# Kernel optimization log

Measured on AMD Instinct MI355X. Metric: run time of the kernel, lower is better.

The kernel has to match this reference:

```python
import jax, jax.numpy as jnp
import numpy as np
import math

SR = 96000.0
FRAME = 2048
NB = 16
GAIN_RANGE = (-24.0, 24.0)
Q_RANGE = (0.5, 16.0)
BROADBAND = (-60.0, 0.0)
HPF_R = (20.0, 500.0)
LPF_R = (5000.0, 20000.0)
SHELF_R = (50.0, 16000.0)
PEAK_R = (100.0, 15000.0)


def _dfreq(n, rng):
    lo, hi = math.log(rng[0]), math.log(rng[1])
    return jnp.exp(lo + n * (hi - lo))


def _dgain(n, rng=GAIN_RANGE):
    return rng[0] + n * (rng[1] - rng[0])


def _dq(n):
    lo, hi = math.log(Q_RANGE[0]), math.log(Q_RANGE[1])
    return jnp.exp(lo + n * (hi - lo))


def _coeffs(ftype, fc, gain_db, Q):
    # returns stacked [g, k, a1, a2, a3, m0, m1, m2], each same shape as fc
    g = jnp.clip(jnp.tan(math.pi * fc / SR), 1e-6, 100.0)
    Q = jnp.clip(Q, 0.1, 100.0)
    one = jnp.ones_like(g)
    zero = jnp.zeros_like(g)
    if ftype in ('highpass', 'lowpass'):
        k = 1.0 / Q
        a1 = 1.0 / (1.0 + g * (g + k)); a2 = g * a1; a3 = g * a2
        if ftype == 'highpass':
            m0, m1, m2 = one, -k, -one
        else:
            m0, m1, m2 = zero, zero, one
    elif ftype == 'peak':
        A = jnp.power(10.0, gain_db / 40.0)
        k = jnp.where(gain_db >= 0, 1.0 / (Q * A), A / Q)
        a1 = 1.0 / (1.0 + g * (g + k)); a2 = g * a1; a3 = g * a2
        m0, m1, m2 = one, k * (A * A - 1.0), zero
    elif ftype == 'lowshelf':
        A = jnp.power(10.0, gain_db / 40.0); sA = jnp.sqrt(A); k = 1.0 / Q
        gs = jnp.where(gain_db >= 0, g / sA, g * sA)
        a1 = 1.0 / (1.0 + gs * (gs + k)); a2 = gs * a1; a3 = gs * a2
        m0, m1, m2 = one, k * (A - 1.0), A * A - 1.0
    else:  # highshelf
        A = jnp.power(10.0, gain_db / 40.0); sA = jnp.sqrt(A); k = 1.0 / Q
        gs = jnp.where(gain_db >= 0, g * sA, g / sA)
        a1 = 1.0 / (1.0 + gs * (gs + k)); a2 = gs * a1; a3 = gs * a2
        m0, m1, m2 = A * A, k * (1.0 - A) * A, 1.0 - A * A
    return jnp.stack([g, k, a1, a2, a3, m0, m1, m2], 0)


def _all_coeffs(params, n_frames_audio):
    # params: (B, 50, n_frames_params) -> coeffs (nF, NB, 8, B), in/out gains (nF, B)
    B = params.shape[0]
    nFp = params.shape[2]
    pidx = jnp.minimum(jnp.arange(n_frames_audio), nFp - 1)
    fp = jnp.take(params, pidx, axis=2)                 # (B, 50, nF)
    bq = fp[:, :NB * 3, :].reshape(B, NB, 3, n_frames_audio)
    in_g = jnp.power(10.0, _dgain(fp[:, -2, :], BROADBAND) / 20.0)   # (B, nF)
    out_g = jnp.power(10.0, _dgain(fp[:, -1, :], BROADBAND) / 20.0)  # (B, nF)
    cs = []
    for i in range(NB):
        fn, gn, qn = bq[:, i, 0], bq[:, i, 1], bq[:, i, 2]  # (B, nF)
        Q = _dq(qn)
        if i == 0:
            c = _coeffs('highpass', _dfreq(fn, HPF_R), None, Q)
        elif i == 15:
            c = _coeffs('lowpass', _dfreq(fn, LPF_R), None, Q)
        elif i == 1:
            c = _coeffs('lowshelf', _dfreq(fn, SHELF_R), _dgain(gn), Q)
        elif i == 14:
            c = _coeffs('highshelf', _dfreq(fn, SHELF_R), _dgain(gn), Q)
        else:
            c = _coeffs('peak', _dfreq(fn, PEAK_R), _dgain(gn), Q)
        cs.append(c)  # (8, B, nF)
    coeffs = jnp.transpose(jnp.stack(cs, 0), (3, 0, 1, 2))  # (nF, NB, 8, B)
    return coeffs, in_g.T, out_g.T


def _forward(audio, params):
    B, S = audio.shape
    nF = S // FRAME  # S chosen as exact multiple of FRAME
    coeffs, in_g, out_g = _all_coeffs(params, nF)
    frames = jnp.transpose(audio.reshape(B, nF, FRAME), (1, 2, 0))  # (nF, FRAME, B)

    def frame_step(states, xs):
        fr, c, ig, og = xs  # fr (FRAME,B), c (NB,8,B), ig (B,), og (B,)
        x = fr * ig[None, :]
        new_states = []
        for i in range(NB):
            a1, a2, a3 = c[i, 2], c[i, 3], c[i, 4]
            m0, m1, m2 = c[i, 5], c[i, 6], c[i, 7]

            def samp(st, xn, a1=a1, a2=a2, a3=a3, m0=m0, m1=m1, m2=m2):
                ic1, ic2 = st
                v3 = xn - ic2
                v1 = a1 * ic1 + a2 * v3
                v2 = ic2 + a2 * v1 + a3 * v3
                out = m0 * xn + m1 * v1 + m2 * v2
                return (2.0 * v1 - ic1, 2.0 * v2 - ic2), out

            (ic1, ic2), x = jax.lax.scan(samp, (states[i, 0], states[i, 1]), x)
            new_states.append(jnp.stack([ic1, ic2], 0))
        return jnp.stack(new_states, 0), x * og[None, :]

    init = jnp.zeros((NB, 2, B), audio.dtype)
    _, out = jax.lax.scan(frame_step, init, (frames, coeffs, in_g, out_g))
    return jnp.transpose(out, (2, 0, 1)).reshape(B, S)  # (B, S)


_forward_jit = jax.jit(_forward)


def setup_inputs() -> dict:
    key = jax.random.key(0)
    k1, k2 = jax.random.split(key)
    B, S, nFp = 32, 49152, 24  # 24 frames of 2048 samples
    audio = jax.random.normal(k1, (B, S), dtype=jnp.float32) * 0.1
    params = jax.random.uniform(k2, (B, 50, nFp), dtype=jnp.float32)
    return {'audio': audio, 'params': params}


def reference(audio, params):
    return _forward_jit(audio, params)
```

## Files before the change

### kernel.cpp

```cpp
#include <hip/hip_runtime.h>
#include <math.h>

#define NBATCH 32
#define S      49152
#define NF     24
#define NB     16
#define NBLK   4
#define CHUNK  16
#define NCH    768
#define NWAVE  12

__device__ __forceinline__ float clampf(float x, float lo, float hi) {
    return fminf(fmaxf(x, lo), hi);
}

#define FOREACH_S(OP) \
    OP(s00) OP(s01) OP(s02) OP(s03) OP(s04) OP(s05) OP(s06) OP(s07) \
    OP(s08) OP(s09) OP(s10) OP(s11) OP(s12) OP(s13) OP(s14) OP(s15)

#define DECL_S(x) float x;

#define STEPA(x) { \
    const float n1_ = fmaf(t00, ic1, fmaf(t01, ic2, b0 * (x))); \
    const float n2_ = fmaf(t10, ic1, fmaf(t11, ic2, b1 * (x))); \
    ic1 = n1_; ic2 = n2_; }

#define STEPC(x) { \
    const float y_  = fmaf(c0, ic1, fmaf(c1, ic2, c2 * (x))); \
    const float n1_ = fmaf(t00, ic1, fmaf(t01, ic2, b0 * (x))); \
    const float n2_ = fmaf(t10, ic1, fmaf(t11, ic2, b1 * (x))); \
    (x) = y_; ic1 = n1_; ic2 = n2_; }

__global__ __launch_bounds__(NCH, 3)
void biquad_chain_kernel(const float* __restrict__ audio,
                         const float* __restrict__ params,
                         float* __restrict__ out,
                         unsigned int* __restrict__ ws)
{
    __shared__ float sc[NB][NF][16];
    __shared__ float sgain[2][NF];
    __shared__ float4 sincl[NB][NWAVE][2];
    __shared__ unsigned int stag[NB][NWAVE];

    const int t       = threadIdx.x;
    const int xcd     = blockIdx.x & 7;
    const int slot_   = blockIdx.x >> 3;
    const int bt      = xcd * 4 + (slot_ & 3);
    const int quarter = slot_ >> 2;
    const int lane    = t & 63;
    const int wave    = t >> 6;
    const int frame   = quarter * 6 + (wave >> 1);

    if (t < NB * NF) {
        const int f  = t / NF;
        const int fr = t % NF;
        const float* P = params + (size_t)bt * 50 * NF;
        const float fn = P[(3 * f + 0) * NF + fr];
        const float gn = P[(3 * f + 1) * NF + fr];
        const float qn = P[(3 * f + 2) * NF + fr];

        float Q = __expf(-0.69314718f + qn * 3.4657359f);
        Q = clampf(Q, 0.1f, 100.0f);

        float lo, hi;
        int type;
        if      (f == 0)  { lo = 20.0f;   hi = 500.0f;   type = 0; }
        else if (f == 15) { lo = 5000.0f; hi = 20000.0f; type = 1; }
        else if (f == 1)  { lo = 50.0f;   hi = 16000.0f; type = 3; }
        else if (f == 14) { lo = 50.0f;   hi = 16000.0f; type = 4; }
        else              { lo = 100.0f;  hi = 15000.0f; type = 2; }

        const float fc = __expf(__logf(lo) + fn * (__logf(hi) - __logf(lo)));
        float g_ = __tanf((float)M_PI * fc / 96000.0f);
        g_ = clampf(g_, 1e-6f, 100.0f);
        const float gdb = -24.0f + 48.0f * gn;

        float a1, a2, a3, m0, m1, m2;
        if (type == 0 || type == 1) {
            const float k = 1.0f / Q;
            a1 = 1.0f / (1.0f + g_ * (g_ + k)); a2 = g_ * a1; a3 = g_ * a2;
            if (type == 0) { m0 = 1.0f; m1 = -k;   m2 = -1.0f; }
            else           { m0 = 0.0f; m1 = 0.0f; m2 = 1.0f;  }
        } else if (type == 2) {
            const float A = __expf(gdb * (2.30258509f / 40.0f));
            const float k = (gdb >= 0.0f) ? 1.0f / (Q * A) : A / Q;
            a1 = 1.0f / (1.0f + g_ * (g_ + k)); a2 = g_ * a1; a3 = g_ * a2;
            m0 = 1.0f; m1 = k * (A * A - 1.0f); m2 = 0.0f;
        } else {
            const float A  = __expf(gdb * (2.30258509f / 40.0f));
            const float sA = sqrtf(A);
            const float k  = 1.0f / Q;
            float gs;
            if (type == 3) gs = (gdb >= 0.0f) ? g_ / sA : g_ * sA;
            else           gs = (gdb >= 0.0f) ? g_ * sA : g_ / sA;
            a1 = 1.0f / (1.0f + gs * (gs + k)); a2 = gs * a1; a3 = gs * a2;
            if (type == 3) { m0 = 1.0f;  m1 = k * (A - 1.0f);      m2 = A * A - 1.0f; }
            else           { m0 = A * A; m1 = k * (1.0f - A) * A;  m2 = 1.0f - A * A; }
        }

        const float q2  = a2 * a2 + a3;
        const float t00 = 2.0f * a1 - 1.0f;
        const float t01 = -2.0f * a2;
        const float t10 = 2.0f * a1 * a2;
        const float t11 = 1.0f - 2.0f * q2;
        const float b0  = 2.0f * a2;
        const float b1  = 2.0f * q2;
        const float c0  = a1 * (m1 + m2 * a2);
        const float c1  = m2 * (1.0f - q2) - m1 * a2;
        const float c2  = m0 + m1 * a2 + m2 * q2;

        float u00 = t00, u01 = t01, u10 = t10, u11 = t11;
        #pragma unroll
        for (int i = 0; i < 4; i++) {
            const float n00 = u00 * u00 + u01 * u10;
            const float n01 = u00 * u01 + u01 * u11;
            const float n10 = u10 * u00 + u11 * u10;
            const float n11 = u10 * u01 + u11 * u11;
            u00 = n00; u01 = n01; u10 = n10; u11 = n11;
        }

        sc[f][fr][0] = t00; sc[f][fr][1] = t01; sc[f][fr][2] = t10; sc[f][fr][3] = t11;
        sc[f][fr][4] = b0;  sc[f][fr][5] = b1;  sc[f][fr][6] = c0;  sc[f][fr][7] = c1;
        sc[f][fr][8] = c2;  sc[f][fr][9] = u00; sc[f][fr][10] = u01; sc[f][fr][11] = u10;
        sc[f][fr][12] = u11;
    }
    if (t >= 384 && t < 384 + 2 * NF) {
        const int idx = t - 384;
        const int which = idx / NF;
        const int fr    = idx % NF;
        const float* P = params + (size_t)bt * 50 * NF;
        const float p  = P[(48 + which) * NF + fr];
        const float db = -60.0f + 60.0f * p;
        sgain[which][fr] = __expf(db * (2.30258509f / 20.0f));
    }
    if (t < NB * NWAVE) stag[t / NWAVE][t % NWAVE] = 0u;
    __syncthreads();

    FOREACH_S(DECL_S)
    {
        const float ing = sgain[0][frame];
        const float* base = audio + (size_t)bt * S
                          + (size_t)(quarter * NCH + t) * CHUNK;
        float4 q;
        q = *(const float4*)(base +  0); s00 = q.x*ing; s01 = q.y*ing; s02 = q.z*ing; s03 = q.w*ing;
        q = *(const float4*)(base +  4); s04 = q.x*ing; s05 = q.y*ing; s06 = q.z*ing; s07 = q.w*ing;
        q = *(const float4*)(base +  8); s08 = q.x*ing; s09 = q.y*ing; s10 = q.z*ing; s11 = q.w*ing;
        q = *(const float4*)(base + 12); s12 = q.x*ing; s13 = q.y*ing; s14 = q.z*ing; s15 = q.w*ing;
    }

    #pragma unroll 1
    for (int f = 0; f < NB; f++) {
        const float4 q0 = *(const float4*)&sc[f][frame][0];
        const float4 q1 = *(const float4*)&sc[f][frame][4];
        const float4 q2 = *(const float4*)&sc[f][frame][8];
        const float  M11v = sc[f][frame][12];
        const float t00 = q0.x, t01 = q0.y, t10 = q0.z, t11 = q0.w;
        const float b0  = q1.x, b1  = q1.y, c0  = q1.z, c1  = q1.w;
        const float c2  = q2.x;

        float ic1 = 0.0f, ic2 = 0.0f;
        FOREACH_S(STEPA)

        float Md00 = q2.y, Md01 = q2.z, Md10 = q2.w, Md11 = M11v;
        float Ac0 = ic1, Ac1 = ic2;
        #pragma unroll
        for (int d = 1; d < 64; d <<= 1) {
            const float lc0 = __shfl_up(Ac0, d);
            const float lc1 = __shfl_up(Ac1, d);
            if (lane >= d) {
                Ac0 = fmaf(Md00, lc0, fmaf(Md01, lc1, Ac0));
                Ac1 = fmaf(Md10, lc0, fmaf(Md11, lc1, Ac1));
            }
            const float n00 = Md00 * Md00 + Md01 * Md10;
            const float n01 = Md00 * Md01 + Md01 * Md11;
            const float n10 = Md10 * Md00 + Md11 * Md10;
            const float n11 = Md10 * Md01 + Md11 * Md11;
            Md00 = n00; Md01 = n01; Md10 = n10; Md11 = n11;
        }

        float ce0 = __shfl_up(Ac0, 1);
        float ce1 = __shfl_up(Ac1, 1);
        if (lane == 0) { ce0 = 0.0f; ce1 = 0.0f; }

        const unsigned int tag = (unsigned int)(f + 1);
        float Mp00 = 1.0f, Mp01 = 0.0f, Mp10 = 0.0f, Mp11 = 1.0f;
        float cp0 = 0.0f, cp1 = 0.0f;
        if (wave > 0) {
            while (__hip_atomic_load(&stag[f][wave - 1], __ATOMIC_ACQUIRE,
                                     __HIP_MEMORY_SCOPE_WORKGROUP) != tag)
                __builtin_amdgcn_s_sleep(1);
            const float4 d0 = sincl[f][wave - 1][0];
            const float4 d1 = sincl[f][wave - 1][1];
            Mp00 = d0.x; Mp01 = d0.y; Mp10 = d0.z; Mp11 = d0.w;
            cp0 = d1.x; cp1 = d1.y;
        } else if (quarter > 0) {
            unsigned int* gs = ws + ((size_t)(bt * NB + f) * NBLK + (quarter - 1)) * 8;
            while (__hip_atomic_load(gs, __ATOMIC_ACQUIRE,
                                     __HIP_MEMORY_SCOPE_AGENT) != tag)
                __builtin_amdgcn_s_sleep(1);
            const float* dp = (const float*)(gs + 1);
            Mp00 = __hip_atomic_load(&dp[0], __ATOMIC_RELAXED, __HIP_MEMORY_SCOPE_AGENT);
            Mp01 = __hip_atomic_load(&dp[1], __ATOMIC_RELAXED, __HIP_MEMORY_SCOPE_AGENT);
            Mp10 = __hip_atomic_load(&dp[2], __ATOMIC_RELAXED, __HIP_MEMORY_SCOPE_AGENT);
            Mp11 = __hip_atomic_load(&dp[3], __ATOMIC_RELAXED, __HIP_MEMORY_SCOPE_AGENT);
            cp0  = __hip_atomic_load(&dp[4], __ATOMIC_RELAXED, __HIP_MEMORY_SCOPE_AGENT);
            cp1  = __hip_atomic_load(&dp[5], __ATOMIC_RELAXED, __HIP_MEMORY_SCOPE_AGENT);
        }

        if (lane == 63) {
            const float I00 = fmaf(Md00, Mp00, Md01 * Mp10);
            const float I01 = fmaf(Md00, Mp01, Md01 * Mp11);
            const float I10 = fmaf(Md10, Mp00, Md11 * Mp10);
            const float I11 = fmaf(Md10, Mp01, Md11 * Mp11);
            const float Ic0 = fmaf(Md00, cp0, fmaf(Md01, cp1, Ac0));
            const float Ic1 = fmaf(Md10, cp0, fmaf(Md11, cp1, Ac1));
            if (wave < NWAVE - 1) {
                sincl[f][wave][0] = make_float4(I00, I01, I10, I11);
                sincl[f][wave][1] = make_float4(Ic0, Ic1, 0.0f, 0.0f);
                __hip_atomic_store(&stag[f][wave], tag, __ATOMIC_RELEASE,
                                   __HIP_MEMORY_SCOPE_WORKGROUP);
            } else if (quarter < NBLK - 1) {
                unsigned int* gs = ws + ((size_t)(bt * NB + f) * NBLK + quarter) * 8;
                float* dp = (float*)(gs + 1);
                __hip_atomic_store(&dp[0], I00, __ATOMIC_RELAXED, __HIP_MEMORY_SCOPE_AGENT);
                __hip_atomic_store(&dp[1], I01, __ATOMIC_RELAXED, __HIP_MEMORY_SCOPE_AGENT);
                __hip_atomic_store(&dp[2], I10, __ATOMIC_RELAXED, __HIP_MEMORY_SCOPE_AGENT);
                __hip_atomic_store(&dp[3], I11, __ATOMIC_RELAXED, __HIP_MEMORY_SCOPE_AGENT);
                __hip_atomic_store(&dp[4], Ic0, __ATOMIC_RELAXED, __HIP_MEMORY_SCOPE_AGENT);
                __hip_atomic_store(&dp[5], Ic1, __ATOMIC_RELAXED, __HIP_MEMORY_SCOPE_AGENT);
                __hip_atomic_store(gs, tag, __ATOMIC_RELEASE, __HIP_MEMORY_SCOPE_AGENT);
            }
        }

        float w0 = cp0, w1 = cp1;
        float p00 = q2.y, p01 = q2.z, p10 = q2.w, p11 = M11v;
        #pragma unroll
        for (int b = 0; b < 6; b++) {
            if (lane & (1 << b)) {
                const float nw0 = fmaf(p00, w0, p01 * w1);
                const float nw1 = fmaf(p10, w0, p11 * w1);
                w0 = nw0; w1 = nw1;
            }
            if (b < 5) {
                const float n00 = p00 * p00 + p01 * p10;
                const float n01 = p00 * p01 + p01 * p11;
                const float n10 = p10 * p00 + p11 * p10;
                const float n11 = p10 * p01 + p11 * p11;
                p00 = n00; p01 = n01; p10 = n10; p11 = n11;
            }
        }
        ic1 = w0 + ce0;
        ic2 = w1 + ce1;

        FOREACH_S(STEPC)
    }

    {
        const float og = sgain[1][frame];
        float* base = out + (size_t)bt * S + (size_t)(quarter * NCH + t) * CHUNK;
        float4 q;
        q.x = s00*og; q.y = s01*og; q.z = s02*og; q.w = s03*og; *(float4*)(base +  0) = q;
        q.x = s04*og; q.y = s05*og; q.z = s06*og; q.w = s07*og; *(float4*)(base +  4) = q;
        q.x = s08*og; q.y = s09*og; q.z = s10*og; q.w = s11*og; *(float4*)(base +  8) = q;
        q.x = s12*og; q.y = s13*og; q.z = s14*og; q.w = s15*og; *(float4*)(base + 12) = q;
    }
}

extern "C" void kernel_launch(void* const* d_in, const int* in_sizes, int n_in,
                              void* d_out, int out_size, void* d_ws, size_t ws_size,
                              hipStream_t stream)
{
    const float* audio  = (const float*)d_in[0];
    const float* params = (const float*)d_in[1];
    float* out = (float*)d_out;
    unsigned int* ws = (unsigned int*)d_ws;
    biquad_chain_kernel<<<NBLK * NBATCH, NCH, 0, stream>>>(audio, params, out, ws);
}
```

Before: 123.1 us.

## Replace serial wave/block carry chain with decoupled aggregate lookback scan

Each wave now publishes only its local affine aggregate (matrix plus offset) to shared memory, then folds all earlier waves' aggregates itself. The previous scheme waited on the predecessor's inclusive prefix, which serialised the chain across waves. Across blocks, the last wave publishes the block aggregate and wave 0 of later blocks folds all preceding blocks' aggregates, then shares the resulting state with its other waves. This is meant to cut the serial dependency latency at the cost of redundant matrix folds, more polling, and the inter-block chain still being waited on.

```diff
diff --git a/kernel.cpp b/kernel.cpp
--- a/kernel.cpp
+++ b/kernel.cpp
@@ -39,8 +39,11 @@
 {
     __shared__ float sc[NB][NF][16];
     __shared__ float sgain[2][NF];
-    __shared__ float4 sincl[NB][NWAVE][2];
-    __shared__ unsigned int stag[NB][NWAVE];
+    __shared__ float4 swaggM[NB][NWAVE];
+    __shared__ float2 swaggC[NB][NWAVE];
+    __shared__ unsigned int swtag[NB][NWAVE];
+    __shared__ float2 sblk[NB];
+    __shared__ unsigned int sblktag[NB];
 
     const int t       = threadIdx.x;
     const int xcd     = blockIdx.x & 7;
@@ -133,7 +136,8 @@
         const float db = -60.0f + 60.0f * p;
         sgain[which][fr] = __expf(db * (2.30258509f / 20.0f));
     }
-    if (t < NB * NWAVE) stag[t / NWAVE][t % NWAVE] = 0u;
+    if (t < NB * NWAVE) swtag[t / NWAVE][t % NWAVE] = 0u;
+    if (t < NB) sblktag[t] = 0u;
     __syncthreads();
 
     FOREACH_S(DECL_S)
@@ -183,56 +187,89 @@
         if (lane == 0) { ce0 = 0.0f; ce1 = 0.0f; }
 
         const unsigned int tag = (unsigned int)(f + 1);
-        float Mp00 = 1.0f, Mp01 = 0.0f, Mp10 = 0.0f, Mp11 = 1.0f;
-        float cp0 = 0.0f, cp1 = 0.0f;
-        if (wave > 0) {
-            while (__hip_atomic_load(&stag[f][wave - 1], __ATOMIC_ACQUIRE,
+
+        if (lane == 63) {
+            swaggM[f][wave] = make_float4(Md00, Md01, Md10, Md11);
+            swaggC[f][wave] = make_float2(Ac0, Ac1);
+            __hip_atomic_store(&swtag[f][wave], tag, __ATOMIC_RELEASE,
+                               __HIP_MEMORY_SCOPE_WORKGROUP);
+        }
+
+        float F00 = 1.0f, F01 = 0.0f, F10 = 0.0f, F11 = 1.0f;
+        float Fc0 = 0.0f, Fc1 = 0.0f;
+        for (int j = 0; j < wave; j++) {
+            while (__hip_atomic_load(&swtag[f][j], __ATOMIC_ACQUIRE,
                                      __HIP_MEMORY_SCOPE_WORKGROUP) != tag)
                 __builtin_amdgcn_s_sleep(1);
-            const float4 d0 = sincl[f][wave - 1][0];
-            const float4 d1 = sincl[f][wave - 1][1];
-            Mp00 = d0.x; Mp01 = d0.y; Mp10 = d0.z; Mp11 = d0.w;
-            cp0 = d1.x; cp1 = d1.y;
-        } else if (quarter > 0) {
-            unsigned int* gs = ws + ((size_t)(bt * NB + f) * NBLK + (quarter - 1)) * 8;
-            while (__hip_atomic_load(gs, __ATOMIC_ACQUIRE,
-                                     __HIP_MEMORY_SCOPE_AGENT) != tag)
-                __builtin_amdgcn_s_sleep(1);
-            const float* dp = (const float*)(gs + 1);
-            Mp00 = __hip_atomic_load(&dp[0], __ATOMIC_RELAXED, __HIP_MEMORY_SCOPE_AGENT);
-            Mp01 = __hip_atomic_load(&dp[1], __ATOMIC_RELAXED, __HIP_MEMORY_SCOPE_AGENT);
-            Mp10 = __hip_atomic_load(&dp[2], __ATOMIC_RELAXED, __HIP_MEMORY_SCOPE_AGENT);
-            Mp11 = __hip_atomic_load(&dp[3], __ATOMIC_RELAXED, __HIP_MEMORY_SCOPE_AGENT);
-            cp0  = __hip_atomic_load(&dp[4], __ATOMIC_RELAXED, __HIP_MEMORY_SCOPE_AGENT);
-            cp1  = __hip_atomic_load(&dp[5], __ATOMIC_RELAXED, __HIP_MEMORY_SCOPE_AGENT);
-        }
-
-        if (lane == 63) {
-            const float I00 = fmaf(Md00, Mp00, Md01 * Mp10);
-            const float I01 = fmaf(Md00, Mp01, Md01 * Mp11);
-            const float I10 = fmaf(Md10, Mp00, Md11 * Mp10);
-            const float I11 = fmaf(Md10, Mp01, Md11 * Mp11);
-            const float Ic0 = fmaf(Md00, cp0, fmaf(Md01, cp1, Ac0));
-            const float Ic1 = fmaf(Md10, cp0, fmaf(Md11, cp1, Ac1));
-            if (wave < NWAVE - 1) {
-                sincl[f][wave][0] = make_float4(I00, I01, I10, I11);
-                sincl[f][wave][1] = make_float4(Ic0, Ic1, 0.0f, 0.0f);
-                __hip_atomic_store(&stag[f][wave], tag, __ATOMIC_RELEASE,
-                                   __HIP_MEMORY_SCOPE_WORKGROUP);
-            } else if (quarter < NBLK - 1) {
+            const float4 m = swaggM[f][j];
+            const float2 c = swaggC[f][j];
+            const float n00 = fmaf(m.x, F00, m.y * F10);
+            const float n01 = fmaf(m.x, F01, m.y * F11);
+            const float n10 = fmaf(m.z, F00, m.w * F10);
+            const float n11 = fmaf(m.z, F01, m.w * F11);
+            const float nc0 = fmaf(m.x, Fc0, fmaf(m.y, Fc1, c.x));
+            const float nc1 = fmaf(m.z, Fc0, fmaf(m.w, Fc1, c.y));
+            F00 = n00; F01 = n01; F10 = n10; F11 = n11;
+            Fc0 = nc0; Fc1 = nc1;
+        }
+
+        if (wave == NWAVE - 1 && quarter < NBLK - 1) {
+            const float B00 = fmaf(Md00, F00, Md01 * F10);
+            const float B01 = fmaf(Md00, F01, Md01 * F11);
+            const float B10 = fmaf(Md10, F00, Md11 * F10);
+            const float B11 = fmaf(Md10, F01, Md11 * F11);
+            const float Bc0 = fmaf(Md00, Fc0, fmaf(Md01, Fc1, Ac0));
+            const float Bc1 = fmaf(Md10, Fc0, fmaf(Md11, Fc1, Ac1));
+            if (lane == 63) {
                 unsigned int* gs = ws + ((size_t)(bt * NB + f) * NBLK + quarter) * 8;
                 float* dp = (float*)(gs + 1);
-                __hip_atomic_store(&dp[0], I00, __ATOMIC_RELAXED, __HIP_MEMORY_SCOPE_AGENT);
-                __hip_atomic_store(&dp[1], I01, __ATOMIC_RELAXED, __HIP_MEMORY_SCOPE_AGENT);
-                __hip_atomic_store(&dp[2], I10, __ATOMIC_RELAXED, __HIP_MEMORY_SCOPE_AGENT);
-                __hip_atomic_store(&dp[3], I11, __ATOMIC_RELAXED, __HIP_MEMORY_SCOPE_AGENT);
-                __hip_atomic_store(&dp[4], Ic0, __ATOMIC_RELAXED, __HIP_MEMORY_SCOPE_AGENT);
-                __hip_atomic_store(&dp[5], Ic1, __ATOMIC_RELAXED, __HIP_MEMORY_SCOPE_AGENT);
+                __hip_atomic_store(&dp[0], B00, __ATOMIC_RELAXED, __HIP_MEMORY_SCOPE_AGENT);
+                __hip_atomic_store(&dp[1], B01, __ATOMIC_RELAXED, __HIP_MEMORY_SCOPE_AGENT);
+                __hip_atomic_store(&dp[2], B10, __ATOMIC_RELAXED, __HIP_MEMORY_SCOPE_AGENT);
+                __hip_atomic_store(&dp[3], B11, __ATOMIC_RELAXED, __HIP_MEMORY_SCOPE_AGENT);
+                __hip_atomic_store(&dp[4], Bc0, __ATOMIC_RELAXED, __HIP_MEMORY_SCOPE_AGENT);
+                __hip_atomic_store(&dp[5], Bc1, __ATOMIC_RELAXED, __HIP_MEMORY_SCOPE_AGENT);
                 __hip_atomic_store(gs, tag, __ATOMIC_RELEASE, __HIP_MEMORY_SCOPE_AGENT);
             }
         }
 
-        float w0 = cp0, w1 = cp1;
+        float Sbx = 0.0f, Sby = 0.0f;
+        if (quarter > 0) {
+            if (wave == 0) {
+                for (int k = 0; k < quarter; k++) {
+                    unsigned int* gs = ws + ((size_t)(bt * NB + f) * NBLK + k) * 8;
+                    while (__hip_atomic_load(gs, __ATOMIC_ACQUIRE,
+                                             __HIP_MEMORY_SCOPE_AGENT) != tag)
+                        __builtin_amdgcn_s_sleep(1);
+                    const float* dp = (const float*)(gs + 1);
+                    const float m00 = __hip_atomic_load(&dp[0], __ATOMIC_RELAXED, __HIP_MEMORY_SCOPE_AGENT);
+                    const float m01 = __hip_atomic_load(&dp[1], __ATOMIC_RELAXED, __HIP_MEMORY_SCOPE_AGENT);
+                    const float m10 = __hip_atomic_load(&dp[2], __ATOMIC_RELAXED, __HIP_MEMORY_SCOPE_AGENT);
+                    const float m11 = __hip_atomic_load(&dp[3], __ATOMIC_RELAXED, __HIP_MEMORY_SCOPE_AGENT);
+                    const float cc0 = __hip_atomic_load(&dp[4], __ATOMIC_RELAXED, __HIP_MEMORY_SCOPE_AGENT);
+                    const float cc1 = __hip_atomic_load(&dp[5], __ATOMIC_RELAXED, __HIP_MEMORY_SCOPE_AGENT);
+                    const float nx = fmaf(m00, Sbx, fmaf(m01, Sby, cc0));
+                    const float ny = fmaf(m10, Sbx, fmaf(m11, Sby, cc1));
+                    Sbx = nx; Sby = ny;
+                }
+                if (lane == 0) {
+                    sblk[f] = make_float2(Sbx, Sby);
+                    __hip_atomic_store(&sblktag[f], tag, __ATOMIC_RELEASE,
+                                       __HIP_MEMORY_SCOPE_WORKGROUP);
+                }
+            } else {
+                while (__hip_atomic_load(&sblktag[f], __ATOMIC_ACQUIRE,
+                                         __HIP_MEMORY_SCOPE_WORKGROUP) != tag)
+                    __builtin_amdgcn_s_sleep(1);
+                const float2 sb = sblk[f];
+                Sbx = sb.x; Sby = sb.y;
+            }
+        }
+
+        const float vx = fmaf(F00, Sbx, fmaf(F01, Sby, Fc0));
+        const float vy = fmaf(F10, Sbx, fmaf(F11, Sby, Fc1));
+
+        float w0 = vx, w1 = vy;
         float p00 = q2.y, p01 = q2.z, p10 = q2.w, p11 = M11v;
         #pragma unroll
         for (int b = 0; b < 6; b++) {
```

Result: slower. 138.2 us (+12.3%).

## Map one wave per frame and pass only state vectors between frames

Applied to the files above, without the earlier changes.

Restructures the chunked-scan biquad kernel so each wave handles one whole 2048-sample frame (32 samples per lane), with 4 waves per block and 6 blocks per batch item. Each block now computes coefficients only for its own 4 frames. Because coefficients change at frame boundaries, only the 2-element state needs to pass between waves and blocks, so the 2x2 transfer-matrix composition and the larger handoff payloads go away. In exchange, each lane holds more registers for 32 samples, the serial sequential work per lane doubles, and the cross-block dependency chain gets longer (6 blocks instead of 4).

```diff
diff --git a/kernel.cpp b/kernel.cpp
--- a/kernel.cpp
+++ b/kernel.cpp
@@ -5,10 +5,10 @@
 #define S      49152
 #define NF     24
 #define NB     16
-#define NBLK   4
-#define CHUNK  16
-#define NCH    768
-#define NWAVE  12
+#define CHUNK  32
+#define NWPB   4
+#define NBLKF  6
+#define NCH    256
 
 __device__ __forceinline__ float clampf(float x, float lo, float hi) {
     return fminf(fmaxf(x, lo), hi);
@@ -16,7 +16,9 @@
 
 #define FOREACH_S(OP) \
     OP(s00) OP(s01) OP(s02) OP(s03) OP(s04) OP(s05) OP(s06) OP(s07) \
-    OP(s08) OP(s09) OP(s10) OP(s11) OP(s12) OP(s13) OP(s14) OP(s15)
+    OP(s08) OP(s09) OP(s10) OP(s11) OP(s12) OP(s13) OP(s14) OP(s15) \
+    OP(s16) OP(s17) OP(s18) OP(s19) OP(s20) OP(s21) OP(s22) OP(s23) \
+    OP(s24) OP(s25) OP(s26) OP(s27) OP(s28) OP(s29) OP(s30) OP(s31)
 
 #define DECL_S(x) float x;
 
@@ -31,87 +33,94 @@
     const float n2_ = fmaf(t10, ic1, fmaf(t11, ic2, b1 * (x))); \
     (x) = y_; ic1 = n1_; ic2 = n2_; }
 
-__global__ __launch_bounds__(NCH, 3)
+struct Aff { float t00, t01, t10, t11, b0, b1, c0, c1, c2; };
+
+__device__ __forceinline__ Aff biquad_affine(int f, const float* P, int fr) {
+    const float fn = P[(3 * f + 0) * NF + fr];
+    const float gn = P[(3 * f + 1) * NF + fr];
+    const float qn = P[(3 * f + 2) * NF + fr];
+
+    float Q = __expf(-0.69314718f + qn * 3.4657359f);
+    Q = clampf(Q, 0.1f, 100.0f);
+
+    float lo, hi;
+    int type;
+    if      (f == 0)  { lo = 20.0f;   hi = 500.0f;   type = 0; }
+    else if (f == 15) { lo = 5000.0f; hi = 20000.0f; type = 1; }
+    else if (f == 1)  { lo = 50.0f;   hi = 16000.0f; type = 3; }
+    else if (f == 14) { lo = 50.0f;   hi = 16000.0f; type = 4; }
+    else              { lo = 100.0f;  hi = 15000.0f; type = 2; }
+
+    const float fc = __expf(__logf(lo) + fn * (__logf(hi) - __logf(lo)));
+    float g_ = __tanf((float)M_PI * fc / 96000.0f);
+    g_ = clampf(g_, 1e-6f, 100.0f);
+    const float gdb = -24.0f + 48.0f * gn;
+
+    float a1, a2, a3, m0, m1, m2;
+    if (type == 0 || type == 1) {
+        const float k = 1.0f / Q;
+        a1 = 1.0f / (1.0f + g_ * (g_ + k)); a2 = g_ * a1; a3 = g_ * a2;
+        if (type == 0) { m0 = 1.0f; m1 = -k;   m2 = -1.0f; }
+        else           { m0 = 0.0f; m1 = 0.0f; m2 = 1.0f;  }
+    } else if (type == 2) {
+        const float A = __expf(gdb * (2.30258509f / 40.0f));
+        const float k = (gdb >= 0.0f) ? 1.0f / (Q * A) : A / Q;
+        a1 = 1.0f / (1.0f + g_ * (g_ + k)); a2 = g_ * a1; a3 = g_ * a2;
+        m0 = 1.0f; m1 = k * (A * A - 1.0f); m2 = 0.0f;
+    } else {
+        const float A  = __expf(gdb * (2.30258509f / 40.0f));
+        const float sA = sqrtf(A);
+        const float k  = 1.0f / Q;
+        float gs;
+        if (type == 3) gs = (gdb >= 0.0f) ? g_ / sA : g_ * sA;
+        else           gs = (gdb >= 0.0f) ? g_ * sA : g_ / sA;
+        a1 = 1.0f / (1.0f + gs * (gs + k)); a2 = gs * a1; a3 = gs * a2;
+        if (type == 3) { m0 = 1.0f;  m1 = k * (A - 1.0f);      m2 = A * A - 1.0f; }
+        else           { m0 = A * A; m1 = k * (1.0f - A) * A;  m2 = 1.0f - A * A; }
+    }
+
+    const float q2 = a2 * a2 + a3;
+    Aff r;
+    r.t00 = 2.0f * a1 - 1.0f;
+    r.t01 = -2.0f * a2;
+    r.t10 = 2.0f * a1 * a2;
+    r.t11 = 1.0f - 2.0f * q2;
+    r.b0  = 2.0f * a2;
+    r.b1  = 2.0f * q2;
+    r.c0  = a1 * (m1 + m2 * a2);
+    r.c1  = m2 * (1.0f - q2) - m1 * a2;
+    r.c2  = m0 + m1 * a2 + m2 * q2;
+    return r;
+}
+
+__global__ __launch_bounds__(NCH, 2)
 void biquad_chain_kernel(const float* __restrict__ audio,
                          const float* __restrict__ params,
                          float* __restrict__ out,
                          unsigned int* __restrict__ ws)
 {
-    __shared__ float sc[NB][NF][16];
-    __shared__ float sgain[2][NF];
-    __shared__ float4 sincl[NB][NWAVE][2];
-    __shared__ unsigned int stag[NB][NWAVE];
-
-    const int t       = threadIdx.x;
-    const int xcd     = blockIdx.x & 7;
-    const int slot_   = blockIdx.x >> 3;
-    const int bt      = xcd * 4 + (slot_ & 3);
-    const int quarter = slot_ >> 2;
-    const int lane    = t & 63;
-    const int wave    = t >> 6;
-    const int frame   = quarter * 6 + (wave >> 1);
-
-    if (t < NB * NF) {
-        const int f  = t / NF;
-        const int fr = t % NF;
+    __shared__ float scf[NWPB][NB][16];
+    __shared__ float sgain[2][NWPB];
+    __shared__ float sst[NWPB - 1][NB][2];
+    __shared__ unsigned int stag[NWPB - 1][NB];
+
+    const int t    = threadIdx.x;
+    const int bt   = blockIdx.x & 31;
+    const int blk  = blockIdx.x >> 5;
+    const int lane = t & 63;
+    const int wave = t >> 6;
+    const int frg  = blk * NWPB + wave;
+
+    if (t < NWPB * NB) {
+        const int f   = t & 15;
+        const int frl = t >> 4;
+        const int fr  = blk * NWPB + frl;
         const float* P = params + (size_t)bt * 50 * NF;
-        const float fn = P[(3 * f + 0) * NF + fr];
-        const float gn = P[(3 * f + 1) * NF + fr];
-        const float qn = P[(3 * f + 2) * NF + fr];
-
-        float Q = __expf(-0.69314718f + qn * 3.4657359f);
-        Q = clampf(Q, 0.1f, 100.0f);
-
-        float lo, hi;
-        int type;
-        if      (f == 0)  { lo = 20.0f;   hi = 500.0f;   type = 0; }
-        else if (f == 15) { lo = 5000.0f; hi = 20000.0f; type = 1; }
-        else if (f == 1)  { lo = 50.0f;   hi = 16000.0f; type = 3; }
-        else if (f == 14) { lo = 50.0f;   hi = 16000.0f; type = 4; }
-        else              { lo = 100.0f;  hi = 15000.0f; type = 2; }
-
-        const float fc = __expf(__logf(lo) + fn * (__logf(hi) - __logf(lo)));
-        float g_ = __tanf((float)M_PI * fc / 96000.0f);
-        g_ = clampf(g_, 1e-6f, 100.0f);
-        const float gdb = -24.0f + 48.0f * gn;
-
-        float a1, a2, a3, m0, m1, m2;
-        if (type == 0 || type == 1) {
-            const float k = 1.0f / Q;
-            a1 = 1.0f / (1.0f + g_ * (g_ + k)); a2 = g_ * a1; a3 = g_ * a2;
-            if (type == 0) { m0 = 1.0f; m1 = -k;   m2 = -1.0f; }
-            else           { m0 = 0.0f; m1 = 0.0f; m2 = 1.0f;  }
-        } else if (type == 2) {
-            const float A = __expf(gdb * (2.30258509f / 40.0f));
-            const float k = (gdb >= 0.0f) ? 1.0f / (Q * A) : A / Q;
-            a1 = 1.0f / (1.0f + g_ * (g_ + k)); a2 = g_ * a1; a3 = g_ * a2;
-            m0 = 1.0f; m1 = k * (A * A - 1.0f); m2 = 0.0f;
-        } else {
-            const float A  = __expf(gdb * (2.30258509f / 40.0f));
-            const float sA = sqrtf(A);
-            const float k  = 1.0f / Q;
-            float gs;
-            if (type == 3) gs = (gdb >= 0.0f) ? g_ / sA : g_ * sA;
-            else           gs = (gdb >= 0.0f) ? g_ * sA : g_ / sA;
-            a1 = 1.0f / (1.0f + gs * (gs + k)); a2 = gs * a1; a3 = gs * a2;
-            if (type == 3) { m0 = 1.0f;  m1 = k * (A - 1.0f);      m2 = A * A - 1.0f; }
-            else           { m0 = A * A; m1 = k * (1.0f - A) * A;  m2 = 1.0f - A * A; }
-        }
-
-        const float q2  = a2 * a2 + a3;
-        const float t00 = 2.0f * a1 - 1.0f;
-        const float t01 = -2.0f * a2;
-        const float t10 = 2.0f * a1 * a2;
-        const float t11 = 1.0f - 2.0f * q2;
-        const float b0  = 2.0f * a2;
-        const float b1  = 2.0f * q2;
-        const float c0  = a1 * (m1 + m2 * a2);
-        const float c1  = m2 * (1.0f - q2) - m1 * a2;
-        const float c2  = m0 + m1 * a2 + m2 * q2;
-
-        float u00 = t00, u01 = t01, u10 = t10, u11 = t11;
+        const Aff A = biquad_affine(f, P, fr);
+
+        float u00 = A.t00, u01 = A.t01, u10 = A.t10, u11 = A.t11;
         #pragma unroll
-        for (int i = 0; i < 4; i++) {
+        for (int i = 0; i < 5; i++) {
             const float n00 = u00 * u00 + u01 * u10;
             const float n01 = u00 * u01 + u01 * u11;
             const float n10 = u10 * u00 + u11 * u10;
@@ -119,41 +128,48 @@
             u00 = n00; u01 = n01; u10 = n10; u11 = n11;
         }
 
-        sc[f][fr][0] = t00; sc[f][fr][1] = t01; sc[f][fr][2] = t10; sc[f][fr][3] = t11;
-        sc[f][fr][4] = b0;  sc[f][fr][5] = b1;  sc[f][fr][6] = c0;  sc[f][fr][7] = c1;
-        sc[f][fr][8] = c2;  sc[f][fr][9] = u00; sc[f][fr][10] = u01; sc[f][fr][11] = u10;
-        sc[f][fr][12] = u11;
-    }
-    if (t >= 384 && t < 384 + 2 * NF) {
-        const int idx = t - 384;
-        const int which = idx / NF;
-        const int fr    = idx % NF;
-        const float* P = params + (size_t)bt * 50 * NF;
-        const float p  = P[(48 + which) * NF + fr];
-        const float db = -60.0f + 60.0f * p;
-        sgain[which][fr] = __expf(db * (2.30258509f / 20.0f));
-    }
-    if (t < NB * NWAVE) stag[t / NWAVE][t % NWAVE] = 0u;
+        float* d = scf[frl][f];
+        d[0] = A.t00; d[1] = A.t01; d[2]  = A.t10; d[3]  = A.t11;
+        d[4] = A.b0;  d[5] = A.b1;  d[6]  = A.c0;  d[7]  = A.c1;
+        d[8] = A.c2;  d[9] = u00;   d[10] = u01;   d[11] = u10;
+        d[12] = u11;
+    }
+    if (t >= 64 && t < 64 + 2 * NWPB) {
+        const int idx   = t - 64;
+        const int which = idx >> 2;
+        const int frl   = idx & 3;
+        const int fr    = blk * NWPB + frl;
+        const float* P  = params + (size_t)bt * 50 * NF;
+        const float p   = P[(48 + which) * NF + fr];
+        const float db  = -60.0f + 60.0f * p;
+        sgain[which][frl] = __expf(db * (2.30258509f / 20.0f));
+    }
+    if (t < (NWPB - 1) * NB) stag[t / NB][t % NB] = 0u;
     __syncthreads();
 
     FOREACH_S(DECL_S)
     {
-        const float ing = sgain[0][frame];
-        const float* base = audio + (size_t)bt * S
-                          + (size_t)(quarter * NCH + t) * CHUNK;
+        const float ing = sgain[0][wave];
+        const float* base = audio + (size_t)bt * S + (size_t)frg * 2048
+                          + (size_t)lane * CHUNK;
         float4 q;
         q = *(const float4*)(base +  0); s00 = q.x*ing; s01 = q.y*ing; s02 = q.z*ing; s03 = q.w*ing;
         q = *(const float4*)(base +  4); s04 = q.x*ing; s05 = q.y*ing; s06 = q.z*ing; s07 = q.w*ing;
         q = *(const float4*)(base +  8); s08 = q.x*ing; s09 = q.y*ing; s10 = q.z*ing; s11 = q.w*ing;
         q = *(const float4*)(base + 12); s12 = q.x*ing; s13 = q.y*ing; s14 = q.z*ing; s15 = q.w*ing;
+        q = *(const float4*)(base + 16); s16 = q.x*ing; s17 = q.y*ing; s18 = q.z*ing; s19 = q.w*ing;
+        q = *(const float4*)(base + 20); s20 = q.x*ing; s21 = q.y*ing; s22 = q.z*ing; s23 = q.w*ing;
+        q = *(const float4*)(base + 24); s24 = q.x*ing; s25 = q.y*ing; s26 = q.z*ing; s27 = q.w*ing;
+        q = *(const float4*)(base + 28); s28 = q.x*ing; s29 = q.y*ing; s30 = q.z*ing; s31 = q.w*ing;
     }
 
     #pragma unroll 1
     for (int f = 0; f < NB; f++) {
-        const float4 q0 = *(const float4*)&sc[f][frame][0];
-        const float4 q1 = *(const float4*)&sc[f][frame][4];
-        const float4 q2 = *(const float4*)&sc[f][frame][8];
-        const float  M11v = sc[f][frame][12];
+        const float* d = scf[wave][f];
+        const float4 q0 = *(const float4*)(d + 0);
+        const float4 q1 = *(const float4*)(d + 4);
+        const float4 q2 = *(const float4*)(d + 8);
+        const float  M11v = d[12];
         const float t00 = q0.x, t01 = q0.y, t10 = q0.z, t11 = q0.w;
         const float b0  = q1.x, b1  = q1.y, c0  = q1.z, c1  = q1.w;
         const float c2  = q2.x;
@@ -164,10 +180,10 @@
         float Md00 = q2.y, Md01 = q2.z, Md10 = q2.w, Md11 = M11v;
         float Ac0 = ic1, Ac1 = ic2;
         #pragma unroll
-        for (int d = 1; d < 64; d <<= 1) {
-            const float lc0 = __shfl_up(Ac0, d);
-            const float lc1 = __shfl_up(Ac1, d);
-            if (lane >= d) {
+        for (int dd = 1; dd < 64; dd <<= 1) {
+            const float lc0 = __shfl_up(Ac0, dd);
+            const float lc1 = __shfl_up(Ac1, dd);
+            if (lane >= dd) {
                 Ac0 = fmaf(Md00, lc0, fmaf(Md01, lc1, Ac0));
                 Ac1 = fmaf(Md10, lc0, fmaf(Md11, lc1, Ac1));
             }
@@ -183,56 +199,47 @@
         if (lane == 0) { ce0 = 0.0f; ce1 = 0.0f; }
 
         const unsigned int tag = (unsigned int)(f + 1);
-        float Mp00 = 1.0f, Mp01 = 0.0f, Mp10 = 0.0f, Mp11 = 1.0f;
-        float cp0 = 0.0f, cp1 = 0.0f;
-        if (wave > 0) {
-            while (__hip_atomic_load(&stag[f][wave - 1], __ATOMIC_ACQUIRE,
-                                     __HIP_MEMORY_SCOPE_WORKGROUP) != tag)
-                __builtin_amdgcn_s_sleep(1);
-            const float4 d0 = sincl[f][wave - 1][0];
-            const float4 d1 = sincl[f][wave - 1][1];
-            Mp00 = d0.x; Mp01 = d0.y; Mp10 = d0.z; Mp11 = d0.w;
-            cp0 = d1.x; cp1 = d1.y;
-        } else if (quarter > 0) {
-            unsigned int* gs = ws + ((size_t)(bt * NB + f) * NBLK + (quarter - 1)) * 8;
-            while (__hip_atomic_load(gs, __ATOMIC_ACQUIRE,
-                                     __HIP_MEMORY_SCOPE_AGENT) != tag)
-                __builtin_amdgcn_s_sleep(1);
-            const float* dp = (const float*)(gs + 1);
-            Mp00 = __hip_atomic_load(&dp[0], __ATOMIC_RELAXED, __HIP_MEMORY_SCOPE_AGENT);
-            Mp01 = __hip_atomic_load(&dp[1], __ATOMIC_RELAXED, __HIP_MEMORY_SCOPE_AGENT);
-            Mp10 = __hip_atomic_load(&dp[2], __ATOMIC_RELAXED, __HIP_MEMORY_SCOPE_AGENT);
-            Mp11 = __hip_atomic_load(&dp[3], __ATOMIC_RELAXED, __HIP_MEMORY_SCOPE_AGENT);
-            cp0  = __hip_atomic_load(&dp[4], __ATOMIC_RELAXED, __HIP_MEMORY_SCOPE_AGENT);
-            cp1  = __hip_atomic_load(&dp[5], __ATOMIC_RELAXED, __HIP_MEMORY_SCOPE_AGENT);
-        }
-
-        if (lane == 63) {
-            const float I00 = fmaf(Md00, Mp00, Md01 * Mp10);
-            const float I01 = fmaf(Md00, Mp01, Md01 * Mp11);
-            const float I10 = fmaf(Md10, Mp00, Md11 * Mp10);
-            const float I11 = fmaf(Md10, Mp01, Md11 * Mp11);
-            const float Ic0 = fmaf(Md00, cp0, fmaf(Md01, cp1, Ac0));
-            const float Ic1 = fmaf(Md10, cp0, fmaf(Md11, cp1, Ac1));
-            if (wave < NWAVE - 1) {
-                sincl[f][wave][0] = make_float4(I00, I01, I10, I11);
-                sincl[f][wave][1] = make_float4(Ic0, Ic1, 0.0f, 0.0f);
-                __hip_atomic_store(&stag[f][wave], tag, __ATOMIC_RELEASE,
+        float v0 = 0.0f, v1 = 0.0f;
+        if (frg > 0) {
+            if (wave > 0) {
+                while (__hip_atomic_load(&stag[wave - 1][f], __ATOMIC_ACQUIRE,
+                                         __HIP_MEMORY_SCOPE_WORKGROUP) != tag)
+                    __builtin_amdgcn_s_sleep(1);
+                v0 = sst[wave - 1][f][0];
+                v1 = sst[wave - 1][f][1];
+            } else {
+                unsigned int* gs = ws + ((size_t)(bt * (NBLKF - 1) + (blk - 1)) * NB + f) * 4;
+                if (lane == 0) {
+                    while (__hip_atomic_load(gs, __ATOMIC_ACQUIRE,
+                                             __HIP_MEMORY_SCOPE_AGENT) != tag)
+                        __builtin_amdgcn_s_sleep(1);
+                    const float* dp = (const float*)(gs + 1);
+                    v0 = __hip_atomic_load(&dp[0], __ATOMIC_RELAXED, __HIP_MEMORY_SCOPE_AGENT);
+                    v1 = __hip_atomic_load(&dp[1], __ATOMIC_RELAXED, __HIP_MEMORY_SCOPE_AGENT);
+                }
+                v0 = __shfl(v0, 0);
+                v1 = __shfl(v1, 0);
+            }
+        }
+
+        if (lane == 63 && frg < NF - 1) {
+            const float o0 = fmaf(Md00, v0, fmaf(Md01, v1, Ac0));
+            const float o1 = fmaf(Md10, v0, fmaf(Md11, v1, Ac1));
+            if (wave < NWPB - 1) {
+                sst[wave][f][0] = o0;
+                sst[wave][f][1] = o1;
+                __hip_atomic_store(&stag[wave][f], tag, __ATOMIC_RELEASE,
                                    __HIP_MEMORY_SCOPE_WORKGROUP);
-            } else if (quarter < NBLK - 1) {
-                unsigned int* gs = ws + ((size_t)(bt * NB + f) * NBLK + quarter) * 8;
+            } else {
+                unsigned int* gs = ws + ((size_t)(bt * (NBLKF - 1) + blk) * NB + f) * 4;
                 float* dp = (float*)(gs + 1);
-                __hip_atomic_store(&dp[0], I00, __ATOMIC_RELAXED, __HIP_MEMORY_SCOPE_AGENT);
-                __hip_atomic_store(&dp[1], I01, __ATOMIC_RELAXED, __HIP_MEMORY_SCOPE_AGENT);
-                __hip_atomic_store(&dp[2], I10, __ATOMIC_RELAXED, __HIP_MEMORY_SCOPE_AGENT);
-                __hip_atomic_store(&dp[3], I11, __ATOMIC_RELAXED, __HIP_MEMORY_SCOPE_AGENT);
-                __hip_atomic_store(&dp[4], Ic0, __ATOMIC_RELAXED, __HIP_MEMORY_SCOPE_AGENT);
-                __hip_atomic_store(&dp[5], Ic1, __ATOMIC_RELAXED, __HIP_MEMORY_SCOPE_AGENT);
+                __hip_atomic_store(&dp[0], o0, __ATOMIC_RELAXED, __HIP_MEMORY_SCOPE_AGENT);
+                __hip_atomic_store(&dp[1], o1, __ATOMIC_RELAXED, __HIP_MEMORY_SCOPE_AGENT);
                 __hip_atomic_store(gs, tag, __ATOMIC_RELEASE, __HIP_MEMORY_SCOPE_AGENT);
             }
         }
 
-        float w0 = cp0, w1 = cp1;
+        float w0 = v0, w1 = v1;
         float p00 = q2.y, p01 = q2.z, p10 = q2.w, p11 = M11v;
         #pragma unroll
         for (int b = 0; b < 6; b++) {
@@ -256,13 +263,18 @@
     }
 
     {
-        const float og = sgain[1][frame];
-        float* base = out + (size_t)bt * S + (size_t)(quarter * NCH + t) * CHUNK;
+        const float og = sgain[1][wave];
+        float* base = out + (size_t)bt * S + (size_t)frg * 2048
+                    + (size_t)lane * CHUNK;
         float4 q;
         q.x = s00*og; q.y = s01*og; q.z = s02*og; q.w = s03*og; *(float4*)(base +  0) = q;
         q.x = s04*og; q.y = s05*og; q.z = s06*og; q.w = s07*og; *(float4*)(base +  4) = q;
         q.x = s08*og; q.y = s09*og; q.z = s10*og; q.w = s11*og; *(float4*)(base +  8) = q;
         q.x = s12*og; q.y = s13*og; q.z = s14*og; q.w = s15*og; *(float4*)(base + 12) = q;
+        q.x = s16*og; q.y = s17*og; q.z = s18*og; q.w = s19*og; *(float4*)(base + 16) = q;
+        q.x = s20*og; q.y = s21*og; q.z = s22*og; q.w = s23*og; *(float4*)(base + 20) = q;
+        q.x = s24*og; q.y = s25*og; q.z = s26*og; q.w = s27*og; *(float4*)(base + 24) = q;
+        q.x = s28*og; q.y = s29*og; q.z = s30*og; q.w = s31*og; *(float4*)(base + 28) = q;
     }
 }
 
@@ -274,5 +286,5 @@
     const float* params = (const float*)d_in[1];
     float* out = (float*)d_out;
     unsigned int* ws = (unsigned int*)d_ws;
-    biquad_chain_kernel<<<NBLK * NBATCH, NCH, 0, stream>>>(audio, params, out, ws);
-}
+    biquad_chain_kernel<<<NBLKF * NBATCH, NCH, 0, stream>>>(audio, params, out, ws);
+}
```

After: 147.4 us. +19.8%, slower.

## Replace serial wave-chained state scan with precomputed transition matrices and single-wave combine

Applied to the files above, without the earlier changes.

Precomputes per-wave and per-quarter transition-matrix powers in shared memory during setup, so the per-filter cross-wave combine becomes a block barrier plus one wave doing a short serial affine scan over the wave aggregates. Blocks now publish only a 2-float carry vector instead of a full matrix plus vector, and each block reads all earlier blocks' carries in parallel instead of waiting on a chain. This removes the wave-to-wave and block-to-block serial spin-wait chain. In exchange it adds a __syncthreads per filter stage, more shared memory and setup work, and it relies on the piecewise-constant frame structure to precompute the matrices.

```diff
diff --git a/kernel.cpp b/kernel.cpp
--- a/kernel.cpp
+++ b/kernel.cpp
@@ -38,9 +38,14 @@
                          unsigned int* __restrict__ ws)
 {
     __shared__ float sc[NB][NF][16];
+    __shared__ float sT2048[NB][NF][4];
+    __shared__ float sMw[NB][NWAVE][4];
+    __shared__ float sPm[NB][NWAVE][4];
+    __shared__ float sWm[NB][3][4];
     __shared__ float sgain[2][NF];
-    __shared__ float4 sincl[NB][NWAVE][2];
-    __shared__ unsigned int stag[NB][NWAVE];
+    __shared__ float sagg[2][NWAVE][2];
+    __shared__ float sv[NWAVE][2];
+    __shared__ unsigned int sflag[NB];
 
     const int t       = threadIdx.x;
     const int xcd     = blockIdx.x & 7;
@@ -118,11 +123,34 @@
             const float n11 = u10 * u01 + u11 * u11;
             u00 = n00; u01 = n01; u10 = n10; u11 = n11;
         }
-
         sc[f][fr][0] = t00; sc[f][fr][1] = t01; sc[f][fr][2] = t10; sc[f][fr][3] = t11;
         sc[f][fr][4] = b0;  sc[f][fr][5] = b1;  sc[f][fr][6] = c0;  sc[f][fr][7] = c1;
         sc[f][fr][8] = c2;  sc[f][fr][9] = u00; sc[f][fr][10] = u01; sc[f][fr][11] = u10;
         sc[f][fr][12] = u11;
+
+        #pragma unroll
+        for (int i = 0; i < 6; i++) {
+            const float n00 = u00 * u00 + u01 * u10;
+            const float n01 = u00 * u01 + u01 * u11;
+            const float n10 = u10 * u00 + u11 * u10;
+            const float n11 = u10 * u01 + u11 * u11;
+            u00 = n00; u01 = n01; u10 = n10; u11 = n11;
+        }
+        const int lf = fr - quarter * 6;
+        if (lf >= 0 && lf < 6) {
+            sMw[f][2 * lf][0] = u00; sMw[f][2 * lf][1] = u01;
+            sMw[f][2 * lf][2] = u10; sMw[f][2 * lf][3] = u11;
+            sMw[f][2 * lf + 1][0] = u00; sMw[f][2 * lf + 1][1] = u01;
+            sMw[f][2 * lf + 1][2] = u10; sMw[f][2 * lf + 1][3] = u11;
+        }
+        {
+            const float n00 = u00 * u00 + u01 * u10;
+            const float n01 = u00 * u01 + u01 * u11;
+            const float n10 = u10 * u00 + u11 * u10;
+            const float n11 = u10 * u01 + u11 * u11;
+            sT2048[f][fr][0] = n00; sT2048[f][fr][1] = n01;
+            sT2048[f][fr][2] = n10; sT2048[f][fr][3] = n11;
+        }
     }
     if (t >= 384 && t < 384 + 2 * NF) {
         const int idx = t - 384;
@@ -133,7 +161,56 @@
         const float db = -60.0f + 60.0f * p;
         sgain[which][fr] = __expf(db * (2.30258509f / 20.0f));
     }
-    if (t < NB * NWAVE) stag[t / NWAVE][t % NWAVE] = 0u;
+    if (t < NB) sflag[t] = 0u;
+    __syncthreads();
+
+    if (t < NB) {
+        const int f = t;
+        float q00 = 1.0f, q01 = 0.0f, q10 = 0.0f, q11 = 1.0f;
+        #pragma unroll
+        for (int k = 0; k < 6; k++) {
+            sPm[f][2 * k][0] = q00; sPm[f][2 * k][1] = q01;
+            sPm[f][2 * k][2] = q10; sPm[f][2 * k][3] = q11;
+            const float m00 = sMw[f][2 * k][0], m01 = sMw[f][2 * k][1];
+            const float m10 = sMw[f][2 * k][2], m11 = sMw[f][2 * k][3];
+            sPm[f][2 * k + 1][0] = m00 * q00 + m01 * q10;
+            sPm[f][2 * k + 1][1] = m00 * q01 + m01 * q11;
+            sPm[f][2 * k + 1][2] = m10 * q00 + m11 * q10;
+            sPm[f][2 * k + 1][3] = m10 * q01 + m11 * q11;
+            const float g00 = sT2048[f][quarter * 6 + k][0], g01 = sT2048[f][quarter * 6 + k][1];
+            const float g10 = sT2048[f][quarter * 6 + k][2], g11 = sT2048[f][quarter * 6 + k][3];
+            const float n00 = g00 * q00 + g01 * q10;
+            const float n01 = g00 * q01 + g01 * q11;
+            const float n10 = g10 * q00 + g11 * q10;
+            const float n11 = g10 * q01 + g11 * q11;
+            q00 = n00; q01 = n01; q10 = n10; q11 = n11;
+        }
+        if (quarter > 0) {
+            float r00 = 1.0f, r01 = 0.0f, r10 = 0.0f, r11 = 1.0f;
+            for (int k = quarter - 1; k >= 0; k--) {
+                sWm[f][k][0] = r00; sWm[f][k][1] = r01;
+                sWm[f][k][2] = r10; sWm[f][k][3] = r11;
+                if (k > 0) {
+                    float b00 = 1.0f, b01 = 0.0f, b10 = 0.0f, b11 = 1.0f;
+                    #pragma unroll
+                    for (int m = 0; m < 6; m++) {
+                        const float g00 = sT2048[f][6 * k + m][0], g01 = sT2048[f][6 * k + m][1];
+                        const float g10 = sT2048[f][6 * k + m][2], g11 = sT2048[f][6 * k + m][3];
+                        const float n00 = g00 * b00 + g01 * b10;
+                        const float n01 = g00 * b01 + g01 * b11;
+                        const float n10 = g10 * b00 + g11 * b10;
+                        const float n11 = g10 * b01 + g11 * b11;
+                        b00 = n00; b01 = n01; b10 = n10; b11 = n11;
+                    }
+                    const float n00 = r00 * b00 + r01 * b10;
+                    const float n01 = r00 * b01 + r01 * b11;
+                    const float n10 = r10 * b00 + r11 * b10;
+                    const float n11 = r10 * b01 + r11 * b11;
+                    r00 = n00; r01 = n01; r10 = n10; r11 = n11;
+                }
+            }
+        }
+    }
     __syncthreads();
 
     FOREACH_S(DECL_S)
@@ -178,61 +255,85 @@
             Md00 = n00; Md01 = n01; Md10 = n10; Md11 = n11;
         }
 
+        const int buf = f & 1;
+        if (lane == 63) {
+            sagg[buf][wave][0] = Ac0;
+            sagg[buf][wave][1] = Ac1;
+        }
+        __syncthreads();
+
+        const unsigned int tag = (unsigned int)(f + 1);
+        unsigned int* stagebase = ws + ((size_t)(bt * NB + f) * NBLK) * 8;
+
+        if (wave == 0) {
+            float Pc0 = 0.0f, Pc1 = 0.0f;
+            #pragma unroll
+            for (int j = 0; j < NWAVE; j++) {
+                const float a0 = sagg[buf][j][0];
+                const float a1v = sagg[buf][j][1];
+                const float m00 = sMw[f][j][0], m01 = sMw[f][j][1];
+                const float m10 = sMw[f][j][2], m11 = sMw[f][j][3];
+                if (lane > j) {
+                    const float n0 = fmaf(m00, Pc0, fmaf(m01, Pc1, a0));
+                    const float n1 = fmaf(m10, Pc0, fmaf(m11, Pc1, a1v));
+                    Pc0 = n0; Pc1 = n1;
+                }
+            }
+
+            if (quarter < NBLK - 1 && lane == NWAVE) {
+                unsigned int* slot = stagebase + quarter * 8;
+                float* dp = (float*)(slot + 1);
+                __hip_atomic_store(&dp[0], Pc0, __ATOMIC_RELAXED, __HIP_MEMORY_SCOPE_AGENT);
+                __hip_atomic_store(&dp[1], Pc1, __ATOMIC_RELAXED, __HIP_MEMORY_SCOPE_AGENT);
+                __hip_atomic_store(slot, tag, __ATOMIC_RELEASE, __HIP_MEMORY_SCOPE_AGENT);
+            }
+
+            float S0x = 0.0f, S0y = 0.0f;
+            if (quarter > 0) {
+                float ux = 0.0f, uy = 0.0f;
+                if (lane < quarter) {
+                    unsigned int* slot = stagebase + lane * 8;
+                    while (__hip_atomic_load(slot, __ATOMIC_ACQUIRE, __HIP_MEMORY_SCOPE_AGENT) != tag) {
+                        __builtin_amdgcn_s_sleep(1);
+                    }
+                    const float* dp = (const float*)(slot + 1);
+                    const float cx = __hip_atomic_load(&dp[0], __ATOMIC_RELAXED, __HIP_MEMORY_SCOPE_AGENT);
+                    const float cy = __hip_atomic_load(&dp[1], __ATOMIC_RELAXED, __HIP_MEMORY_SCOPE_AGENT);
+                    const float w00 = sWm[f][lane][0], w01 = sWm[f][lane][1];
+                    const float w10 = sWm[f][lane][2], w11 = sWm[f][lane][3];
+                    ux = fmaf(w00, cx, w01 * cy);
+                    uy = fmaf(w10, cx, w11 * cy);
+                }
+                S0x = __shfl(ux, 0);
+                S0y = __shfl(uy, 0);
+                if (quarter > 1) { S0x += __shfl(ux, 1); S0y += __shfl(uy, 1); }
+                if (quarter > 2) { S0x += __shfl(ux, 2); S0y += __shfl(uy, 2); }
+            }
+
+            if (lane < NWAVE) {
+                const float p00 = sPm[f][lane][0], p01 = sPm[f][lane][1];
+                const float p10 = sPm[f][lane][2], p11 = sPm[f][lane][3];
+                sv[lane][0] = fmaf(p00, S0x, fmaf(p01, S0y, Pc0));
+                sv[lane][1] = fmaf(p10, S0x, fmaf(p11, S0y, Pc1));
+            }
+            if (lane == 0) {
+                __hip_atomic_store(&sflag[f], tag, __ATOMIC_RELEASE,
+                                   __HIP_MEMORY_SCOPE_WORKGROUP);
+            }
+        } else {
+            while (__hip_atomic_load(&sflag[f], __ATOMIC_ACQUIRE,
+                                     __HIP_MEMORY_SCOPE_WORKGROUP) != tag)
+                __builtin_amdgcn_s_sleep(1);
+        }
+
+        const float vx = sv[wave][0];
+        const float vy = sv[wave][1];
+
         float ce0 = __shfl_up(Ac0, 1);
         float ce1 = __shfl_up(Ac1, 1);
         if (lane == 0) { ce0 = 0.0f; ce1 = 0.0f; }
 
-        const unsigned int tag = (unsigned int)(f + 1);
-        float Mp00 = 1.0f, Mp01 = 0.0f, Mp10 = 0.0f, Mp11 = 1.0f;
-        float cp0 = 0.0f, cp1 = 0.0f;
-        if (wave > 0) {
-            while (__hip_atomic_load(&stag[f][wave - 1], __ATOMIC_ACQUIRE,
-                                     __HIP_MEMORY_SCOPE_WORKGROUP) != tag)
-                __builtin_amdgcn_s_sleep(1);
-            const float4 d0 = sincl[f][wave - 1][0];
-            const float4 d1 = sincl[f][wave - 1][1];
-            Mp00 = d0.x; Mp01 = d0.y; Mp10 = d0.z; Mp11 = d0.w;
-            cp0 = d1.x; cp1 = d1.y;
-        } else if (quarter > 0) {
-            unsigned int* gs = ws + ((size_t)(bt * NB + f) * NBLK + (quarter - 1)) * 8;
-            while (__hip_atomic_load(gs, __ATOMIC_ACQUIRE,
-                                     __HIP_MEMORY_SCOPE_AGENT) != tag)
-                __builtin_amdgcn_s_sleep(1);
-            const float* dp = (const float*)(gs + 1);
-            Mp00 = __hip_atomic_load(&dp[0], __ATOMIC_RELAXED, __HIP_MEMORY_SCOPE_AGENT);
-            Mp01 = __hip_atomic_load(&dp[1], __ATOMIC_RELAXED, __HIP_MEMORY_SCOPE_AGENT);
-            Mp10 = __hip_atomic_load(&dp[2], __ATOMIC_RELAXED, __HIP_MEMORY_SCOPE_AGENT);
-            Mp11 = __hip_atomic_load(&dp[3], __ATOMIC_RELAXED, __HIP_MEMORY_SCOPE_AGENT);
-            cp0  = __hip_atomic_load(&dp[4], __ATOMIC_RELAXED, __HIP_MEMORY_SCOPE_AGENT);
-            cp1  = __hip_atomic_load(&dp[5], __ATOMIC_RELAXED, __HIP_MEMORY_SCOPE_AGENT);
-        }
-
-        if (lane == 63) {
-            const float I00 = fmaf(Md00, Mp00, Md01 * Mp10);
-            const float I01 = fmaf(Md00, Mp01, Md01 * Mp11);
-            const float I10 = fmaf(Md10, Mp00, Md11 * Mp10);
-            const float I11 = fmaf(Md10, Mp01, Md11 * Mp11);
-            const float Ic0 = fmaf(Md00, cp0, fmaf(Md01, cp1, Ac0));
-            const float Ic1 = fmaf(Md10, cp0, fmaf(Md11, cp1, Ac1));
-            if (wave < NWAVE - 1) {
-                sincl[f][wave][0] = make_float4(I00, I01, I10, I11);
-                sincl[f][wave][1] = make_float4(Ic0, Ic1, 0.0f, 0.0f);
-                __hip_atomic_store(&stag[f][wave], tag, __ATOMIC_RELEASE,
-                                   __HIP_MEMORY_SCOPE_WORKGROUP);
-            } else if (quarter < NBLK - 1) {
-                unsigned int* gs = ws + ((size_t)(bt * NB + f) * NBLK + quarter) * 8;
-                float* dp = (float*)(gs + 1);
-                __hip_atomic_store(&dp[0], I00, __ATOMIC_RELAXED, __HIP_MEMORY_SCOPE_AGENT);
-                __hip_atomic_store(&dp[1], I01, __ATOMIC_RELAXED, __HIP_MEMORY_SCOPE_AGENT);
-                __hip_atomic_store(&dp[2], I10, __ATOMIC_RELAXED, __HIP_MEMORY_SCOPE_AGENT);
-                __hip_atomic_store(&dp[3], I11, __ATOMIC_RELAXED, __HIP_MEMORY_SCOPE_AGENT);
-                __hip_atomic_store(&dp[4], Ic0, __ATOMIC_RELAXED, __HIP_MEMORY_SCOPE_AGENT);
-                __hip_atomic_store(&dp[5], Ic1, __ATOMIC_RELAXED, __HIP_MEMORY_SCOPE_AGENT);
-                __hip_atomic_store(gs, tag, __ATOMIC_RELEASE, __HIP_MEMORY_SCOPE_AGENT);
-            }
-        }
-
-        float w0 = cp0, w1 = cp1;
+        float w0 = vx, w1 = vy;
         float p00 = q2.y, p01 = q2.z, p10 = q2.w, p11 = M11v;
         #pragma unroll
         for (int b = 0; b < 6; b++) {
```

Result: no change. 122.4 us (-0.6%).
